# Optimization experiments

Hardware: AMD Instinct MI355X
Metric: run time of the kernel (lower is better)

## Reference

```python
import jax, jax.numpy as jnp
import numpy as np

N_NODES = 100000


def sage_conv(x, src, dst, counts, Wl, bl, Wr):
    # mean-aggregate source features into destination nodes
    msg_sum = jax.ops.segment_sum(x[src], dst, num_segments=N_NODES)  # [N, d]
    aggr = msg_sum / counts  # zero-degree nodes stay 0 (counts clamped to 1)
    return aggr @ Wl + bl + x @ Wr


def setup_inputs() -> dict:
    key = jax.random.key(0)
    ks = jax.random.split(key, 16)
    N, E, IN, H, OUT = N_NODES, 640000, 128, 128, 40
    x = jax.random.normal(ks[0], (N, IN), dtype=jnp.float32)
    edge_index = jax.random.randint(ks[1], (2, E), 0, N, dtype=jnp.int64)

    def lin(k, fan_in, fan_out):
        s = 1.0 / np.sqrt(fan_in)
        return jax.random.uniform(k, (fan_in, fan_out), jnp.float32, -s, s)

    return {
        "x": x,
        "edge_index": edge_index,
        "W1l": lin(ks[2], IN, H), "b1": jnp.zeros((H,), jnp.float32), "W1r": lin(ks[3], IN, H),
        "W2l": lin(ks[4], H, H), "b2": jnp.zeros((H,), jnp.float32), "W2r": lin(ks[5], H, H),
        "W3l": lin(ks[6], H, H), "b3": jnp.zeros((H,), jnp.float32), "W3r": lin(ks[7], H, H),
        "Wf1": lin(ks[8], H, H), "bf1": jnp.zeros((H,), jnp.float32),
        "Wf2": lin(ks[9], H, OUT), "bf2": jnp.zeros((OUT,), jnp.float32),
    }


def reference(x, edge_index, W1l, b1, W1r, W2l, b2, W2r, W3l, b3, W3r, Wf1, bf1, Wf2, bf2):
    src, dst = edge_index[0], edge_index[1]
    counts = jax.ops.segment_sum(jnp.ones_like(dst, dtype=x.dtype), dst,
                                 num_segments=N_NODES)
    counts = jnp.maximum(counts, 1.0)[:, None]  # [N, 1]

    h = jax.nn.relu(sage_conv(x, src, dst, counts, W1l, b1, W1r))
    h = jax.nn.relu(sage_conv(h, src, dst, counts, W2l, b2, W2r))
    h = sage_conv(h, src, dst, counts, W3l, b3, W3r)

    z = jax.nn.relu(h @ Wf1 + bf1) @ Wf2 + bf2  # [N, out]
    return jax.nn.log_softmax(z, axis=1), h
```

## Files before the change

### kernel.cpp

```cpp
#include <hip/hip_runtime.h>
#include <math.h>

#define N_NODES 100000
#define HDIM    128
#define ODIM    40
#define NBLK    ((N_NODES + 255) / 256)

typedef unsigned short u16;
typedef unsigned int   u32;
typedef short bf16x8 __attribute__((ext_vector_type(8)));
typedef float f32x4  __attribute__((ext_vector_type(4)));

__device__ inline float bf16lo_to_f(u32 v) {
    u32 u = v << 16; float f; __builtin_memcpy(&f, &u, 4); return f;
}
__device__ inline float bf16hi_to_f(u32 v) {
    u32 u = v & 0xffff0000u; float f; __builtin_memcpy(&f, &u, 4); return f;
}
__device__ inline u16 f_to_bf16(float f) {
    u32 u; __builtin_memcpy(&u, &f, 4);
    u32 r = (u + 0x7fffu + ((u >> 16) & 1u)) >> 16;
    return (u16)r;
}
__device__ inline u32 pack_bf16x2(float a, float b) {
    return (u32)f_to_bf16(a) | ((u32)f_to_bf16(b) << 16);
}

__global__ __launch_bounds__(256) void count_deg_kernel(
    const int* __restrict__ dst, int* __restrict__ ic, int E)
{
    int e = blockIdx.x * 256 + threadIdx.x;
    if (e < E) atomicAdd(ic + dst[e], 1);
}

__global__ __launch_bounds__(256) void block_sum_kernel(
    const int* __restrict__ ic, int* __restrict__ bs, int n)
{
    __shared__ int sm[256];
    int t = threadIdx.x;
    int i = blockIdx.x * 256 + t;
    sm[t] = (i < n) ? ic[i] : 0;
    __syncthreads();
    for (int s = 128; s > 0; s >>= 1) {
        if (t < s) sm[t] += sm[t + s];
        __syncthreads();
    }
    if (t == 0) bs[blockIdx.x] = sm[0];
}

__global__ __launch_bounds__(512) void scan_bs_kernel(int* __restrict__ bs, int nb)
{
    __shared__ int sm[512];
    int t = threadIdx.x;
    sm[t] = (t < nb) ? bs[t] : 0;
    __syncthreads();
    for (int off = 1; off < 512; off <<= 1) {
        int v = (t >= off) ? sm[t - off] : 0;
        __syncthreads();
        sm[t] += v;
        __syncthreads();
    }
    if (t < nb) bs[t] = (t == 0) ? 0 : sm[t - 1];
}

__global__ __launch_bounds__(256) void scan_block_kernel(
    const int* __restrict__ ic, const int* __restrict__ bs,
    int* __restrict__ pc, int n)
{
    __shared__ int sm[256];
    int t = threadIdx.x;
    int i = blockIdx.x * 256 + t;
    int v = (i < n) ? ic[i] : 0;
    sm[t] = v;
    __syncthreads();
    for (int off = 1; off < 256; off <<= 1) {
        int u = (t >= off) ? sm[t - off] : 0;
        __syncthreads();
        sm[t] += u;
        __syncthreads();
    }
    if (i < n) pc[i] = bs[blockIdx.x] + sm[t] - v;
}

__global__ __launch_bounds__(256) void fill_kernel(
    const int* __restrict__ src, const int* __restrict__ dst,
    int* __restrict__ pc, int* __restrict__ cs, int E)
{
    int e = blockIdx.x * 256 + threadIdx.x;
    if (e < E) {
        int p = atomicAdd(pc + dst[e], 1);
        cs[p] = src[e];
    }
}

__global__ __launch_bounds__(256) void f2bf_kernel(
    const float2* __restrict__ in, u32* __restrict__ out, int n2)
{
    int i = blockIdx.x * 256 + threadIdx.x;
    if (i < n2) { float2 v = in[i]; out[i] = pack_bf16x2(v.x, v.y); }
}

struct WPtrs { const float* w[7]; };

__global__ __launch_bounds__(256) void pack_w_kernel(WPtrs p, u16* __restrict__ out)
{
    int mat = blockIdx.y;
    int e = blockIdx.x * 256 + threadIdx.x;
    int k = e >> 7, n = e & 127;
    float v = p.w[mat][e];
    int nt = n >> 4, ks = k >> 5, q = (k >> 3) & 3, j = k & 7;
    int dst = mat * 16384 + (((nt * 4 + ks) * 64 + q * 16 + (n & 15)) << 3) + j;
    out[dst] = f_to_bf16(v);
}

__global__ __launch_bounds__(256) void pack_wf2_kernel(
    const float* __restrict__ Wf2, u16* __restrict__ outp)
{
    int e = blockIdx.x * 256 + threadIdx.x;
    if (e >= 128 * 48) return;
    int k = e / 48, n = e - k * 48;
    float v = (n < ODIM) ? Wf2[k * ODIM + n] : 0.f;
    int nt = n >> 4, ks = k >> 5, q = (k >> 3) & 3, j = k & 7;
    outp[(((nt * 4 + ks) * 64 + q * 16 + (n & 15)) << 3) + j] = f_to_bf16(v);
}

__global__ __launch_bounds__(256) void gather_mean16_kernel(
    const u32* __restrict__ feat,
    const int* __restrict__ cs, const int* __restrict__ pc, const int* __restrict__ ic,
    u32* __restrict__ A)
{
    const int wave = threadIdx.x >> 6;
    const int lane = threadIdx.x & 63;
    const int node = blockIdx.x * 4 + wave;
    const int end  = pc[node];
    const int deg  = ic[node];
    const int start = end - deg;
    const int g    = lane >> 4;
    const int ch   = lane & 15;

    float acc[8] = {0.f,0.f,0.f,0.f,0.f,0.f,0.f,0.f};

    for (int b = start; b < end; b += 64) {
        int m = end - b; if (m > 64) m = 64;
        int idxv = cs[b + (lane < m ? lane : 0)];
        for (int j = 0; j < m; j += 4) {
            int nb = j + g;
            int s  = __shfl(idxv, nb, 64);
            uint4 v = {0u, 0u, 0u, 0u};
            if (nb < m)
                v = *reinterpret_cast<const uint4*>(feat + ((size_t)s << 6) + (ch << 2));
            acc[0] += bf16lo_to_f(v.x); acc[1] += bf16hi_to_f(v.x);
            acc[2] += bf16lo_to_f(v.y); acc[3] += bf16hi_to_f(v.y);
            acc[4] += bf16lo_to_f(v.z); acc[5] += bf16hi_to_f(v.z);
            acc[6] += bf16lo_to_f(v.w); acc[7] += bf16hi_to_f(v.w);
        }
    }

    #pragma unroll
    for (int off = 16; off < 64; off <<= 1) {
        #pragma unroll
        for (int k = 0; k < 8; ++k) acc[k] += __shfl_xor(acc[k], off, 64);
    }

    if (lane < 16) {
        float inv = 1.0f / (float)(deg > 0 ? deg : 1);
        uint4 o;
        o.x = pack_bf16x2(acc[0] * inv, acc[1] * inv);
        o.y = pack_bf16x2(acc[2] * inv, acc[3] * inv);
        o.z = pack_bf16x2(acc[4] * inv, acc[5] * inv);
        o.w = pack_bf16x2(acc[6] * inv, acc[7] * inv);
        *reinterpret_cast<uint4*>(A + ((size_t)node << 6) + (ch << 2)) = o;
    }
}

__global__ __launch_bounds__(256) void mfma_gemm_kernel(
    const u16* __restrict__ A1, const u16* __restrict__ A2,
    const u16* __restrict__ W1p, const u16* __restrict__ W2p,
    const float* __restrict__ bias,
    u16* __restrict__ out16, float* __restrict__ out32, int do_relu)
{
    __shared__ u16 sAll[2 * 8192];
    const int tid  = threadIdx.x;
    const int base = blockIdx.x * 64;
    const int nmats = (A2 != nullptr) ? 2 : 1;

    for (int mat = 0; mat < nmats; ++mat) {
        const u16* Ain = mat ? A2 : A1;
        u16* sDst = &sAll[mat * 8192];
        for (int it = 0; it < 4; ++it) {
            int c   = it * 256 + tid;
            int row = c >> 4;
            int ch8 = c & 15;
            int rowg = base + row; if (rowg > N_NODES - 1) rowg = N_NODES - 1;
            uint4 v = *reinterpret_cast<const uint4*>(Ain + ((size_t)rowg << 7) + (ch8 << 3));
            int q = ch8 & 3, ks = ch8 >> 2;
            int dc = ((row >> 4) * 4 + ks) * 64 + q * 16 + (row & 15);
            *reinterpret_cast<uint4*>(sDst + (dc << 3)) = v;
        }
    }
    __syncthreads();

    const int wave = tid >> 6;
    const int lane = tid & 63;

    f32x4 acc[8];
    #pragma unroll
    for (int nt = 0; nt < 8; ++nt) acc[nt] = (f32x4){0.f, 0.f, 0.f, 0.f};

    for (int mat = 0; mat < nmats; ++mat) {
        const u16* Wp = mat ? W2p : W1p;
        const u16* sA = &sAll[mat * 8192];
        #pragma unroll
        for (int ks = 0; ks < 4; ++ks) {
            bf16x8 a = *reinterpret_cast<const bf16x8*>(sA + (((wave * 4 + ks) * 64 + lane) << 3));
            #pragma unroll
            for (int nt = 0; nt < 8; ++nt) {
                bf16x8 b = *reinterpret_cast<const bf16x8*>(Wp + (((nt * 4 + ks) * 64 + lane) << 3));
                acc[nt] = __builtin_amdgcn_mfma_f32_16x16x32_bf16(a, b, acc[nt], 0, 0, 0);
            }
        }
    }

    const int m = lane & 15;
    const int q = lane >> 4;
    #pragma unroll
    for (int nt = 0; nt < 8; ++nt) {
        int col = nt * 16 + m;
        float bv = bias[col];
        #pragma unroll
        for (int r = 0; r < 4; ++r) {
            int rowg = base + wave * 16 + q * 4 + r;
            if (rowg >= N_NODES) continue;
            float v = acc[nt][r] + bv;
            if (do_relu) v = fmaxf(v, 0.f);
            if (out16) out16[((size_t)rowg << 7) + col] = f_to_bf16(v);
            if (out32) out32[((size_t)rowg << 7) + col] = v;
        }
    }
}

__global__ __launch_bounds__(256) void mfma_softmax_kernel(
    const u16* __restrict__ t,
    const u16* __restrict__ Wf2p,
    const float* __restrict__ bf2,
    float* __restrict__ out)
{
    __shared__ u16 sA[8192];
    const int tid  = threadIdx.x;
    const int base = blockIdx.x * 64;

    for (int it = 0; it < 4; ++it) {
        int c   = it * 256 + tid;
        int row = c >> 4;
        int ch8 = c & 15;
        int rowg = base + row; if (rowg > N_NODES - 1) rowg = N_NODES - 1;
        uint4 v = *reinterpret_cast<const uint4*>(t + ((size_t)rowg << 7) + (ch8 << 3));
        int q = ch8 & 3, ks = ch8 >> 2;
        int dc = ((row >> 4) * 4 + ks) * 64 + q * 16 + (row & 15);
        *reinterpret_cast<uint4*>(sA + (dc << 3)) = v;
    }
    __syncthreads();

    const int wave = tid >> 6;
    const int lane = tid & 63;

    f32x4 acc[3];
    #pragma unroll
    for (int nt = 0; nt < 3; ++nt) acc[nt] = (f32x4){0.f, 0.f, 0.f, 0.f};

    #pragma unroll
    for (int ks = 0; ks < 4; ++ks) {
        bf16x8 a = *reinterpret_cast<const bf16x8*>(sA + (((wave * 4 + ks) * 64 + lane) << 3));
        #pragma unroll
        for (int nt = 0; nt < 3; ++nt) {
            bf16x8 b = *reinterpret_cast<const bf16x8*>(Wf2p + (((nt * 4 + ks) * 64 + lane) << 3));
            acc[nt] = __builtin_amdgcn_mfma_f32_16x16x32_bf16(a, b, acc[nt], 0, 0, 0);
        }
    }

    const int m = lane & 15;
    const int q = lane >> 4;

    float z[3][4];
    float mx[4] = {-INFINITY, -INFINITY, -INFINITY, -INFINITY};
    #pragma unroll
    for (int nt = 0; nt < 3; ++nt) {
        int col = nt * 16 + m;
        bool valid = (col < ODIM);
        float bv = valid ? bf2[col] : 0.f;
        #pragma unroll
        for (int r = 0; r < 4; ++r) {
            z[nt][r] = acc[nt][r] + bv;
            if (valid) mx[r] = fmaxf(mx[r], z[nt][r]);
        }
    }
    #pragma unroll
    for (int off = 1; off < 16; off <<= 1) {
        #pragma unroll
        for (int r = 0; r < 4; ++r) mx[r] = fmaxf(mx[r], __shfl_xor(mx[r], off, 16));
    }
    float sum[4] = {0.f, 0.f, 0.f, 0.f};
    #pragma unroll
    for (int nt = 0; nt < 3; ++nt) {
        int col = nt * 16 + m;
        if (col < ODIM) {
            #pragma unroll
            for (int r = 0; r < 4; ++r) sum[r] += expf(z[nt][r] - mx[r]);
        }
    }
    #pragma unroll
    for (int off = 1; off < 16; off <<= 1) {
        #pragma unroll
        for (int r = 0; r < 4; ++r) sum[r] += __shfl_xor(sum[r], off, 16);
    }
    float lse[4];
    #pragma unroll
    for (int r = 0; r < 4; ++r) lse[r] = logf(sum[r]) + mx[r];

    #pragma unroll
    for (int nt = 0; nt < 3; ++nt) {
        int col = nt * 16 + m;
        if (col >= ODIM) continue;
        #pragma unroll
        for (int r = 0; r < 4; ++r) {
            int rowg = base + wave * 16 + q * 4 + r;
            if (rowg >= N_NODES) continue;
            out[(size_t)rowg * ODIM + col] = z[nt][r] - lse[r];
        }
    }
}

extern "C" void kernel_launch(void* const* d_in, const int* in_sizes, int n_in,
                              void* d_out, int out_size, void* d_ws, size_t ws_size,
                              hipStream_t stream) {
    const float* x   = (const float*)d_in[0];
    const int*   ei  = (const int*)d_in[1];
    const int E = in_sizes[1] / 2;
    const int* src = ei;
    const int* dst = ei + E;

    const float* W1l = (const float*)d_in[2];
    const float* b1  = (const float*)d_in[3];
    const float* W1r = (const float*)d_in[4];
    const float* W2l = (const float*)d_in[5];
    const float* b2  = (const float*)d_in[6];
    const float* W2r = (const float*)d_in[7];
    const float* W3l = (const float*)d_in[8];
    const float* b3  = (const float*)d_in[9];
    const float* W3r = (const float*)d_in[10];
    const float* Wf1 = (const float*)d_in[11];
    const float* bf1 = (const float*)d_in[12];
    const float* Wf2 = (const float*)d_in[13];
    const float* bf2 = (const float*)d_in[14];

    float* out     = (float*)d_out;
    float* outTail = out + (size_t)N_NODES * ODIM;

    int* ic = (int*)out;
    int* pc = ic + 100352;
    int* bs = pc + 100352;
    int* cs = bs + 1024;

    const size_t FEAT16 = (size_t)N_NODES * HDIM;
    u16* X16  = (u16*)d_ws;
    u16* F16a = X16  + FEAT16;
    u16* F16b = F16a + FEAT16;
    u16* A16  = F16b + FEAT16;
    u16* Wpk  = A16  + FEAT16;
    u16* Wp_1l = Wpk + 0 * 16384;
    u16* Wp_1r = Wpk + 1 * 16384;
    u16* Wp_2l = Wpk + 2 * 16384;
    u16* Wp_2r = Wpk + 3 * 16384;
    u16* Wp_3l = Wpk + 4 * 16384;
    u16* Wp_3r = Wpk + 5 * 16384;
    u16* Wp_f1 = Wpk + 6 * 16384;
    u16* Wf2p  = Wpk + 7 * 16384;

    const int gemmGrid   = (N_NODES + 63) / 64;
    const int gatherGrid = N_NODES / 4;
    const int edgeGrid   = (E + 255) / 256;
    const int cvtGrid    = (N_NODES * HDIM / 2 + 255) / 256;

    hipMemsetAsync(ic, 0, N_NODES * sizeof(int), stream);
    count_deg_kernel<<<edgeGrid, 256, 0, stream>>>(dst, ic, E);
    block_sum_kernel<<<NBLK, 256, 0, stream>>>(ic, bs, N_NODES);
    scan_bs_kernel<<<1, 512, 0, stream>>>(bs, NBLK);
    scan_block_kernel<<<NBLK, 256, 0, stream>>>(ic, bs, pc, N_NODES);
    fill_kernel<<<edgeGrid, 256, 0, stream>>>(src, dst, pc, cs, E);

    f2bf_kernel<<<cvtGrid, 256, 0, stream>>>((const float2*)x, (u32*)X16, N_NODES * HDIM / 2);
    WPtrs wp; wp.w[0] = W1l; wp.w[1] = W1r; wp.w[2] = W2l; wp.w[3] = W2r;
    wp.w[4] = W3l; wp.w[5] = W3r; wp.w[6] = Wf1;
    pack_w_kernel<<<dim3(64, 7), 256, 0, stream>>>(wp, Wpk);
    pack_wf2_kernel<<<24, 256, 0, stream>>>(Wf2, Wf2p);

    gather_mean16_kernel<<<gatherGrid, 256, 0, stream>>>((const u32*)X16, cs, pc, ic, (u32*)A16);
    mfma_gemm_kernel<<<gemmGrid, 256, 0, stream>>>(A16, X16, Wp_1l, Wp_1r, b1, F16a, nullptr, 1);

    gather_mean16_kernel<<<gatherGrid, 256, 0, stream>>>((const u32*)F16a, cs, pc, ic, (u32*)A16);
    mfma_gemm_kernel<<<gemmGrid, 256, 0, stream>>>(A16, F16a, Wp_2l, Wp_2r, b2, F16b, nullptr, 1);

    gather_mean16_kernel<<<gatherGrid, 256, 0, stream>>>((const u32*)F16b, cs, pc, ic, (u32*)A16);
    mfma_gemm_kernel<<<gemmGrid, 256, 0, stream>>>(A16, F16b, Wp_3l, Wp_3r, b3, F16a, outTail, 0);

    mfma_gemm_kernel<<<gemmGrid, 256, 0, stream>>>(F16a, nullptr, Wp_f1, nullptr, bf1, A16, nullptr, 1);

    mfma_softmax_kernel<<<gemmGrid, 256, 0, stream>>>(A16, Wf2p, bf2, out);
}
```

Before: 469.2 us.

## Fuse MLP head GEMMs, async LDS tile staging, coalesce bf16 GEMM output via LDS

Combines the Wf1 GEMM and the Wf2+log_softmax kernel into one head kernel that keeps the hidden activation in LDS, so one kernel launch and a global round trip of a 100000x128 bf16 buffer go away. The A-tile staging in the GEMMs now uses global_load_lds direct-to-LDS loads in place of register loads followed by LDS stores. The GEMM epilogue stages bf16 results in padded LDS and writes them out as 16-byte coalesced rows instead of scattered 2-byte stores. These add extra barriers and rely on the index mapping of the async load matching the MFMA fragment layout.

```diff
diff --git a/kernel.cpp b/kernel.cpp
--- a/kernel.cpp
+++ b/kernel.cpp
@@ -173,35 +173,39 @@
     }
 }
 
+__device__ inline void stage_tile_async(
+    const u16* __restrict__ Ain, u16* __restrict__ sDst,
+    int base, int wave, int lane)
+{
+    #pragma unroll
+    for (int it = 0; it < 4; ++it) {
+        int s   = (wave * 4 + it) * 64 + lane;
+        int row = ((s >> 8) << 4) | (s & 15);
+        int ch8 = (((s >> 6) & 3) << 2) | ((s >> 4) & 3);
+        int rowg = base + row; if (rowg > N_NODES - 1) rowg = N_NODES - 1;
+        __builtin_amdgcn_global_load_lds(
+            (const __attribute__((address_space(1))) void*)(Ain + ((size_t)rowg << 7) + (ch8 << 3)),
+            (__attribute__((address_space(3))) void*)(sDst + ((wave * 4 + it) << 9)),
+            16, 0, 0);
+    }
+}
+
 __global__ __launch_bounds__(256) void mfma_gemm_kernel(
     const u16* __restrict__ A1, const u16* __restrict__ A2,
     const u16* __restrict__ W1p, const u16* __restrict__ W2p,
     const float* __restrict__ bias,
     u16* __restrict__ out16, float* __restrict__ out32, int do_relu)
 {
-    __shared__ u16 sAll[2 * 8192];
+    __shared__ __align__(16) u16 sAll[2 * 8192];
     const int tid  = threadIdx.x;
     const int base = blockIdx.x * 64;
     const int nmats = (A2 != nullptr) ? 2 : 1;
-
-    for (int mat = 0; mat < nmats; ++mat) {
-        const u16* Ain = mat ? A2 : A1;
-        u16* sDst = &sAll[mat * 8192];
-        for (int it = 0; it < 4; ++it) {
-            int c   = it * 256 + tid;
-            int row = c >> 4;
-            int ch8 = c & 15;
-            int rowg = base + row; if (rowg > N_NODES - 1) rowg = N_NODES - 1;
-            uint4 v = *reinterpret_cast<const uint4*>(Ain + ((size_t)rowg << 7) + (ch8 << 3));
-            int q = ch8 & 3, ks = ch8 >> 2;
-            int dc = ((row >> 4) * 4 + ks) * 64 + q * 16 + (row & 15);
-            *reinterpret_cast<uint4*>(sDst + (dc << 3)) = v;
-        }
-    }
-    __syncthreads();
-
     const int wave = tid >> 6;
     const int lane = tid & 63;
+
+    stage_tile_async(A1, &sAll[0], base, wave, lane);
+    if (nmats == 2) stage_tile_async(A2, &sAll[8192], base, wave, lane);
+    __syncthreads();
 
     f32x4 acc[8];
     #pragma unroll
@@ -220,7 +224,9 @@
             }
         }
     }
-
+    __syncthreads();
+
+    u16* sOut = sAll;
     const int m = lane & 15;
     const int q = lane >> 4;
     #pragma unroll
@@ -229,57 +235,87 @@
         float bv = bias[col];
         #pragma unroll
         for (int r = 0; r < 4; ++r) {
-            int rowg = base + wave * 16 + q * 4 + r;
-            if (rowg >= N_NODES) continue;
             float v = acc[nt][r] + bv;
             if (do_relu) v = fmaxf(v, 0.f);
-            if (out16) out16[((size_t)rowg << 7) + col] = f_to_bf16(v);
-            if (out32) out32[((size_t)rowg << 7) + col] = v;
-        }
-    }
-}
-
-__global__ __launch_bounds__(256) void mfma_softmax_kernel(
-    const u16* __restrict__ t,
-    const u16* __restrict__ Wf2p,
-    const float* __restrict__ bf2,
+            int row = wave * 16 + q * 4 + r;
+            sOut[row * 136 + col] = f_to_bf16(v);
+            if (out32) {
+                int rowg = base + row;
+                if (rowg < N_NODES) out32[((size_t)rowg << 7) + col] = v;
+            }
+        }
+    }
+    __syncthreads();
+
+    if (out16) {
+        #pragma unroll
+        for (int it = 0; it < 4; ++it) {
+            int c = it * 256 + tid;
+            int row = c >> 4, ch = c & 15;
+            int rowg = base + row;
+            if (rowg < N_NODES)
+                *reinterpret_cast<uint4*>(out16 + ((size_t)rowg << 7) + (ch << 3)) =
+                    *reinterpret_cast<const uint4*>(sOut + row * 136 + (ch << 3));
+        }
+    }
+}
+
+__global__ __launch_bounds__(256) void mfma_head_kernel(
+    const u16* __restrict__ h3,
+    const u16* __restrict__ Wf1p, const float* __restrict__ bf1,
+    const u16* __restrict__ Wf2p, const float* __restrict__ bf2,
     float* __restrict__ out)
 {
-    __shared__ u16 sA[8192];
+    __shared__ __align__(16) u16 sA[8192];
     const int tid  = threadIdx.x;
     const int base = blockIdx.x * 64;
-
-    for (int it = 0; it < 4; ++it) {
-        int c   = it * 256 + tid;
-        int row = c >> 4;
-        int ch8 = c & 15;
-        int rowg = base + row; if (rowg > N_NODES - 1) rowg = N_NODES - 1;
-        uint4 v = *reinterpret_cast<const uint4*>(t + ((size_t)rowg << 7) + (ch8 << 3));
-        int q = ch8 & 3, ks = ch8 >> 2;
-        int dc = ((row >> 4) * 4 + ks) * 64 + q * 16 + (row & 15);
-        *reinterpret_cast<uint4*>(sA + (dc << 3)) = v;
-    }
-    __syncthreads();
-
     const int wave = tid >> 6;
     const int lane = tid & 63;
 
-    f32x4 acc[3];
-    #pragma unroll
-    for (int nt = 0; nt < 3; ++nt) acc[nt] = (f32x4){0.f, 0.f, 0.f, 0.f};
-
+    stage_tile_async(h3, sA, base, wave, lane);
+    __syncthreads();
+
+    f32x4 acc[8];
+    #pragma unroll
+    for (int nt = 0; nt < 8; ++nt) acc[nt] = (f32x4){0.f, 0.f, 0.f, 0.f};
     #pragma unroll
     for (int ks = 0; ks < 4; ++ks) {
         bf16x8 a = *reinterpret_cast<const bf16x8*>(sA + (((wave * 4 + ks) * 64 + lane) << 3));
         #pragma unroll
+        for (int nt = 0; nt < 8; ++nt) {
+            bf16x8 b = *reinterpret_cast<const bf16x8*>(Wf1p + (((nt * 4 + ks) * 64 + lane) << 3));
+            acc[nt] = __builtin_amdgcn_mfma_f32_16x16x32_bf16(a, b, acc[nt], 0, 0, 0);
+        }
+    }
+    __syncthreads();
+
+    const int m = lane & 15;
+    const int q = lane >> 4;
+    #pragma unroll
+    for (int nt = 0; nt < 8; ++nt) {
+        int col = nt * 16 + m;
+        float bv = bf1[col];
+        #pragma unroll
+        for (int r = 0; r < 4; ++r) {
+            float v = fmaxf(acc[nt][r] + bv, 0.f);
+            int dc = (wave * 4 + (nt >> 1)) * 64 + ((nt & 1) * 2 + (m >> 3)) * 16 + (q * 4 + r);
+            sA[(dc << 3) | (m & 7)] = f_to_bf16(v);
+        }
+    }
+    __syncthreads();
+
+    f32x4 acc2[3];
+    #pragma unroll
+    for (int nt = 0; nt < 3; ++nt) acc2[nt] = (f32x4){0.f, 0.f, 0.f, 0.f};
+    #pragma unroll
+    for (int ks = 0; ks < 4; ++ks) {
+        bf16x8 a = *reinterpret_cast<const bf16x8*>(sA + (((wave * 4 + ks) * 64 + lane) << 3));
+        #pragma unroll
         for (int nt = 0; nt < 3; ++nt) {
             bf16x8 b = *reinterpret_cast<const bf16x8*>(Wf2p + (((nt * 4 + ks) * 64 + lane) << 3));
-            acc[nt] = __builtin_amdgcn_mfma_f32_16x16x32_bf16(a, b, acc[nt], 0, 0, 0);
-        }
-    }
-
-    const int m = lane & 15;
-    const int q = lane >> 4;
+            acc2[nt] = __builtin_amdgcn_mfma_f32_16x16x32_bf16(a, b, acc2[nt], 0, 0, 0);
+        }
+    }
 
     float z[3][4];
     float mx[4] = {-INFINITY, -INFINITY, -INFINITY, -INFINITY};
@@ -290,7 +326,7 @@
         float bv = valid ? bf2[col] : 0.f;
         #pragma unroll
         for (int r = 0; r < 4; ++r) {
-            z[nt][r] = acc[nt][r] + bv;
+            z[nt][r] = acc2[nt][r] + bv;
             if (valid) mx[r] = fmaxf(mx[r], z[nt][r]);
         }
     }
@@ -403,7 +439,5 @@
     gather_mean16_kernel<<<gatherGrid, 256, 0, stream>>>((const u32*)F16b, cs, pc, ic, (u32*)A16);
     mfma_gemm_kernel<<<gemmGrid, 256, 0, stream>>>(A16, F16b, Wp_3l, Wp_3r, b3, F16a, outTail, 0);
 
-    mfma_gemm_kernel<<<gemmGrid, 256, 0, stream>>>(F16a, nullptr, Wp_f1, nullptr, bf1, A16, nullptr, 1);
-
-    mfma_softmax_kernel<<<gemmGrid, 256, 0, stream>>>(A16, Wf2p, bf2, out);
-}
+    mfma_head_kernel<<<gemmGrid, 256, 0, stream>>>(F16a, Wp_f1, bf1, Wf2p, bf2, out);
+}
```

Result: faster. 427.2 us (-8.9%).
